# Kernel optimization log

Hardware: AMD Instinct MI355X
Metric: run time of the kernel (lower is better)

## Reference

```python
import jax, jax.numpy as jnp
import numpy as np
import math

N, M = 512, 31
INP, EMB, ATT = 64, 64, 64
NUM_RELS = 200
SELF_LOOP_IDX = NUM_RELS  # index num_rels is the self-loop relation


def setup_inputs() -> dict:
    key = jax.random.key(0)
    ks = jax.random.split(key, 11)
    s_w = 1.0 / math.sqrt(EMB)
    return {
        "h": jax.random.normal(ks[0], (N, INP), jnp.float32),
        "msg": jax.random.normal(ks[1], (N, M, EMB), jnp.float32),
        "msg_type": jax.random.randint(ks[2], (N, M), 0, NUM_RELS, jnp.int32),
        "r_label_node": jax.random.randint(ks[3], (N,), 0, NUM_RELS, jnp.int32),
        "r_label_msg": jax.random.randint(ks[4], (N, M), 0, NUM_RELS, jnp.int32),
        "W_self": jax.random.normal(ks[5], (INP, EMB), jnp.float32) * s_w,
        "Q": jax.random.normal(ks[6], (NUM_RELS + 1, EMB, ATT), jnp.float32) * s_w,
        "K": jax.random.normal(ks[7], (NUM_RELS + 1, EMB, ATT), jnp.float32) * s_w,
        "V": jax.random.normal(ks[8], (NUM_RELS + 1, EMB, ATT), jnp.float32) * s_w,
        "ffn_w": jax.random.normal(ks[9], (ATT, EMB), jnp.float32) * s_w,
        "ffn_b": jnp.zeros((EMB,), jnp.float32),
    }


def reference(h, msg, msg_type, r_label_node, r_label_msg, W_self, Q, K, V, ffn_w, ffn_b):
    curr = h @ W_self                                        # [N, EMB]
    x = jnp.concatenate([curr[:, None, :], msg], axis=1)     # [N, M+1, EMB]
    qv_idx = jnp.concatenate([r_label_node[:, None], r_label_msg], axis=1)  # [N, M+1]
    self_col = jnp.full((x.shape[0], 1), SELF_LOOP_IDX, msg_type.dtype)
    k_idx = jnp.concatenate([self_col, msg_type], axis=1)    # [N, M+1]
    # relation-indexed per-token projection weights (irregular gather)
    q = jnp.einsum("nme,nmea->nma", x, Q[qv_idx])            # [N, M+1, ATT]
    k = jnp.einsum("nme,nmea->nma", x, K[k_idx])             # [N, M+1, ATT]
    v = jnp.einsum("nme,nmea->nma", x, V[qv_idx])            # [N, M+1, ATT]
    scores = jnp.einsum("nqa,nka->nqk", q, k) / math.sqrt(ATT)
    # NOTE: original code applies softmax over dim=1 (the query axis)
    att = jax.nn.softmax(scores, axis=1)                     # [N, M+1, M+1]
    pooled = jnp.einsum("nqk,nka->nqa", att, v)[:, 0]        # [N, ATT]
    return pooled @ ffn_w + ffn_b                            # [N, EMB]
```

## Files before the change

kernel.cpp:

```cpp
#include <hip/hip_runtime.h>
#include <math.h>

#define NN 512
#define MM 31
#define TT 32
#define EE 64
#define NREL 200
#define NMAT 201
#define SELF_LOOP 200
#define QCAP 192
#define NT 6
#define WSTR 72
#define CPAD 32

typedef short  short8 __attribute__((ext_vector_type(8)));
typedef float  f32x4  __attribute__((ext_vector_type(4)));

__device__ __forceinline__ unsigned short f2bf(float f) {
    union { float f; unsigned int u; } a; a.f = f;
    unsigned int r = a.u + 0x7FFFu + ((a.u >> 16) & 1u);
    return (unsigned short)(r >> 16);
}
__device__ __forceinline__ float bf2f(unsigned short u) {
    union { unsigned int u; float f; } a; a.u = ((unsigned int)u) << 16;
    return a.f;
}

__global__ __launch_bounds__(256) void prep_convert_kernel(
    const float* __restrict__ h, const float* __restrict__ W_self,
    const float* __restrict__ Q, const float* __restrict__ K,
    const float* __restrict__ V,
    const int* __restrict__ msg_type, const int* __restrict__ r_label_node,
    const int* __restrict__ r_label_msg, const float* __restrict__ msg,
    int* __restrict__ cnt_q, int* __restrict__ cnt_k,
    int* __restrict__ list_q, int* __restrict__ list_k,
    unsigned short* __restrict__ wt_q, unsigned short* __restrict__ wt_k,
    unsigned short* __restrict__ wt_v,
    unsigned short* __restrict__ msg_bf, unsigned short* __restrict__ curr_bf,
    unsigned short* __restrict__ k_bf)
{
    const int bid = blockIdx.x, tid = threadIdx.x;

    if (bid < 3 * NMAT) {
        const int r   = bid % NMAT;
        const int mat = bid / NMAT;
        const float* src = (mat == 0 ? Q : mat == 1 ? K : V) + (size_t)r * EE * EE;
        unsigned short* dst = (mat == 0 ? wt_q : mat == 1 ? wt_k : wt_v)
                              + (size_t)r * EE * EE;
        __shared__ unsigned short t_s[EE * WSTR];
        {
            const int e = tid >> 2, aseg = (tid & 3) * 16;
            const float4* s4 = (const float4*)(src + e * EE + aseg);
            float4 f0 = s4[0], f1 = s4[1], f2 = s4[2], f3 = s4[3];
            unsigned short b[16] = {
                f2bf(f0.x), f2bf(f0.y), f2bf(f0.z), f2bf(f0.w),
                f2bf(f1.x), f2bf(f1.y), f2bf(f1.z), f2bf(f1.w),
                f2bf(f2.x), f2bf(f2.y), f2bf(f2.z), f2bf(f2.w),
                f2bf(f3.x), f2bf(f3.y), f2bf(f3.z), f2bf(f3.w) };
            unsigned short* d = &t_s[e * WSTR + aseg];
            *(short8*)d = *(short8*)&b[0];
            *(short8*)(d + 8) = *(short8*)&b[8];
        }
        __syncthreads();
        {
            const int a = tid >> 2, eseg = (tid & 3) * 16;
            unsigned short o[16];
#pragma unroll
            for (int j = 0; j < 16; ++j)
                o[j] = t_s[(eseg + j) * WSTR + a];
            unsigned short* d = dst + a * EE + eseg;
            *(short8*)d = *(short8*)&o[0];
            *(short8*)(d + 8) = *(short8*)&o[8];
        }
        return;
    }

    const int n = bid - 3 * NMAT;

    if (tid < MM) {
        int j  = n * MM + tid;
        int rl = r_label_msg[j];
        int p  = atomicAdd(&cnt_q[rl * CPAD], 1);
        if (p < QCAP) list_q[rl * QCAP + p] = n * TT + tid + 1;
        int mt = msg_type[j];
        int p2 = atomicAdd(&cnt_k[mt * CPAD], 1);
        if (p2 < QCAP) list_k[mt * QCAP + p2] = n * TT + tid + 1;
    } else if (tid == 63) {
        int r = r_label_node[n];
        int p = atomicAdd(&cnt_q[r * CPAD], 1);
        if (p < QCAP) list_q[r * QCAP + p] = n * TT;
    }

    if (tid < MM * EE / 8) {
        const float4* s4 = (const float4*)(msg + (size_t)n * MM * EE) + tid * 2;
        float4 f0 = s4[0], f1 = s4[1];
        unsigned short b[8] = { f2bf(f0.x), f2bf(f0.y), f2bf(f0.z), f2bf(f0.w),
                                f2bf(f1.x), f2bf(f1.y), f2bf(f1.z), f2bf(f1.w) };
        *(short8*)(msg_bf + (size_t)n * MM * EE + tid * 8) = *(short8*)b;
    }

    __shared__ float c_s[EE];
    if (tid < EE) {
        const float* hrow = h + n * EE;
        float acc = 0.f;
#pragma unroll 8
        for (int e = 0; e < EE; ++e)
            acc = fmaf(hrow[e], W_self[e * EE + tid], acc);
        curr_bf[n * EE + tid] = f2bf(acc);
        c_s[tid] = acc;
    }
    __syncthreads();
    if (tid < EE) {
        const float* K200 = K + (size_t)SELF_LOOP * EE * EE;
        float k0 = 0.f;
#pragma unroll 8
        for (int e = 0; e < EE; ++e)
            k0 = fmaf(c_s[e], K200[e * EE + tid], k0);
        k_bf[(size_t)n * TT * EE + tid] = f2bf(k0);
    }
}

__global__ __launch_bounds__(256) void proj_tile_kernel(
    const unsigned short* __restrict__ curr_bf,
    const unsigned short* __restrict__ msg_bf,
    const unsigned short* __restrict__ wt_q,
    const unsigned short* __restrict__ wt_k,
    const unsigned short* __restrict__ wt_v,
    const int* __restrict__ cnt_q, const int* __restrict__ cnt_k,
    const int* __restrict__ list_q, const int* __restrict__ list_k,
    unsigned short* __restrict__ q_bf, unsigned short* __restrict__ k_bf,
    unsigned short* __restrict__ v_bf)
{
    const int r    = blockIdx.x / NT;
    const int tile = blockIdx.x % NT;
    const int tid  = threadIdx.x;
    const int lane = tid & 63;
    const int wave = tid >> 6;
    const int col  = lane & 15;
    const int quad = lane >> 4;

    const int nq = min(cnt_q[r * CPAD], QCAP);
    const int nk = min(cnt_k[r * CPAD], QCAP);
    const int q0 = tile * 32;
    const bool do_q = q0 < nq;
    const bool do_k = q0 < nk;
    if (!do_q && !do_k) return;

    __shared__ unsigned short wq_s[EE * WSTR];
    __shared__ unsigned short wk_s[EE * WSTR];
    __shared__ unsigned short wv_s[EE * WSTR];
    __shared__ unsigned short x_s[64 * WSTR];
    __shared__ int tq_s[32], tk_s[32];

    {
        const int a = tid >> 2, seg = (tid & 3) * 16;
        const size_t go = (size_t)r * EE * EE + a * EE + seg;
        const int lo = a * WSTR + seg;
        if (do_q) {
            short8 w0 = *(const short8*)(wt_q + go);
            short8 w1 = *(const short8*)(wt_q + go + 8);
            *(short8*)&wq_s[lo] = w0; *(short8*)&wq_s[lo + 8] = w1;
            short8 v0 = *(const short8*)(wt_v + go);
            short8 v1 = *(const short8*)(wt_v + go + 8);
            *(short8*)&wv_s[lo] = v0; *(short8*)&wv_s[lo + 8] = v1;
        }
        if (do_k) {
            short8 k0_ = *(const short8*)(wt_k + go);
            short8 k1_ = *(const short8*)(wt_k + go + 8);
            *(short8*)&wk_s[lo] = k0_; *(short8*)&wk_s[lo + 8] = k1_;
        }
    }

    if (tid < 32) {
        tq_s[tid] = (do_q && q0 + tid < nq) ? list_q[r * QCAP + q0 + tid] : -1;
    } else if (tid < 64) {
        int i = tid - 32;
        tk_s[i] = (do_k && q0 + i < nk) ? list_k[r * QCAP + q0 + i] : -1;
    }

    {
        const int row = tid >> 2;
        const int seg = (tid & 3) * 16;
        const bool qside = row < 32;
        const int li = qside ? (q0 + row) : (q0 + row - 32);
        const bool valid = qside ? (do_q && li < nq) : (do_k && li < nk);
        if (valid) {
            int token = qside ? list_q[r * QCAP + li] : list_k[r * QCAP + li];
            int n = token >> 5, t = token & 31;
            const unsigned short* src = (t == 0)
                ? (curr_bf + n * EE)
                : (msg_bf + ((size_t)n * MM + (t - 1)) * EE);
            short8 s0 = *(const short8*)(src + seg);
            short8 s1 = *(const short8*)(src + seg + 8);
            unsigned short* d = &x_s[row * WSTR + seg];
            *(short8*)d = s0; *(short8*)(d + 8) = s1;
        }
    }
    __syncthreads();

    if (do_q) {
        const int mtile = wave & 1;
        const unsigned short* w_s = (wave >> 1) ? wv_s : wq_s;
        unsigned short* outp = (wave >> 1) ? v_bf : q_bf;
        const int m = mtile * 16 + col;
        f32x4 acc[4] = {{0,0,0,0},{0,0,0,0},{0,0,0,0},{0,0,0,0}};
#pragma unroll
        for (int kk = 0; kk < 2; ++kk) {
            short8 af = *(const short8*)&x_s[m * WSTR + kk * 32 + quad * 8];
#pragma unroll
            for (int nt = 0; nt < 4; ++nt) {
                short8 bf = *(const short8*)&w_s[(nt * 16 + col) * WSTR + kk * 32 + quad * 8];
                acc[nt] = __builtin_amdgcn_mfma_f32_16x16x32_bf16(af, bf, acc[nt], 0, 0, 0);
            }
        }
#pragma unroll
        for (int nt = 0; nt < 4; ++nt)
#pragma unroll
            for (int reg = 0; reg < 4; ++reg) {
                int rrow = mtile * 16 + quad * 4 + reg;
                int token = tq_s[rrow];
                if (token >= 0)
                    outp[(size_t)token * EE + nt * 16 + col] = f2bf(acc[nt][reg]);
            }
    }

    if (do_k) {
        const int mtile = wave & 1;
        const int nh = wave >> 1;
        const int m = 32 + mtile * 16 + col;
        f32x4 acc[2] = {{0,0,0,0},{0,0,0,0}};
#pragma unroll
        for (int kk = 0; kk < 2; ++kk) {
            short8 af = *(const short8*)&x_s[m * WSTR + kk * 32 + quad * 8];
#pragma unroll
            for (int j = 0; j < 2; ++j) {
                int nt = nh * 2 + j;
                short8 bf = *(const short8*)&wk_s[(nt * 16 + col) * WSTR + kk * 32 + quad * 8];
                acc[j] = __builtin_amdgcn_mfma_f32_16x16x32_bf16(af, bf, acc[j], 0, 0, 0);
            }
        }
#pragma unroll
        for (int j = 0; j < 2; ++j)
#pragma unroll
            for (int reg = 0; reg < 4; ++reg) {
                int rrow = mtile * 16 + quad * 4 + reg;
                int token = tk_s[rrow];
                if (token >= 0)
                    k_bf[(size_t)token * EE + (nh * 2 + j) * 16 + col] = f2bf(acc[j][reg]);
            }
    }
}

__global__ __launch_bounds__(256) void attn_kernel(
    const unsigned short* __restrict__ q_bf,
    const unsigned short* __restrict__ k_bf,
    const unsigned short* __restrict__ v_bf,
    const float* __restrict__ ffn_w, const float* __restrict__ ffn_b,
    float* __restrict__ out)
{
    const int n = blockIdx.x, tid = threadIdx.x;
    __shared__ float q_s[TT][68], k_s[TT][68], v_s[TT][68];
    __shared__ float s_s[TT][TT + 1];
    __shared__ float att0[TT];
    __shared__ float pooled[EE];

    {
        const int row = tid >> 3, c8 = (tid & 7) * 8;
        const size_t go = (size_t)n * TT * EE + row * EE + c8;
        short8 q8 = *(const short8*)(q_bf + go);
        short8 k8 = *(const short8*)(k_bf + go);
        short8 v8 = *(const short8*)(v_bf + go);
#pragma unroll
        for (int j = 0; j < 8; ++j) {
            q_s[row][c8 + j] = bf2f(((unsigned short*)&q8)[j]);
            k_s[row][c8 + j] = bf2f(((unsigned short*)&k8)[j]);
            v_s[row][c8 + j] = bf2f(((unsigned short*)&v8)[j]);
        }
    }
    __syncthreads();

    {
        const int ki = tid & 31;
        for (int qi = tid >> 5; qi < TT; qi += 8) {
            const float4* qp = (const float4*)&q_s[qi][0];
            const float4* kp = (const float4*)&k_s[ki][0];
            float acc = 0.f;
            for (int e4 = 0; e4 < EE / 4; ++e4) {
                float4 a = qp[e4], b = kp[e4];
                acc += a.x * b.x + a.y * b.y + a.z * b.z + a.w * b.w;
            }
            s_s[qi][ki] = acc * 0.125f;
        }
    }
    __syncthreads();

    if (tid < TT) {
        float mx = -INFINITY;
        for (int qi = 0; qi < TT; ++qi) mx = fmaxf(mx, s_s[qi][tid]);
        float sum = 0.f;
        for (int qi = 0; qi < TT; ++qi) sum += __expf(s_s[qi][tid] - mx);
        att0[tid] = __expf(s_s[0][tid] - mx) / sum;
    }
    __syncthreads();

    if (tid < EE) {
        float acc = 0.f;
        for (int ki = 0; ki < TT; ++ki)
            acc = fmaf(att0[ki], v_s[ki][tid], acc);
        pooled[tid] = acc;
    }
    __syncthreads();

    if (tid < EE) {
        float acc = ffn_b[tid];
        for (int a = 0; a < EE; ++a)
            acc = fmaf(pooled[a], ffn_w[a * EE + tid], acc);
        out[n * EE + tid] = acc;
    }
}

extern "C" void kernel_launch(void* const* d_in, const int* in_sizes, int n_in,
                              void* d_out, int out_size, void* d_ws, size_t ws_size,
                              hipStream_t stream) {
    const float* h            = (const float*)d_in[0];
    const float* msg          = (const float*)d_in[1];
    const int*   msg_type     = (const int*)  d_in[2];
    const int*   r_label_node = (const int*)  d_in[3];
    const int*   r_label_msg  = (const int*)  d_in[4];
    const float* W_self       = (const float*)d_in[5];
    const float* Q            = (const float*)d_in[6];
    const float* K            = (const float*)d_in[7];
    const float* V            = (const float*)d_in[8];
    const float* ffn_w        = (const float*)d_in[9];
    const float* ffn_b        = (const float*)d_in[10];
    float*       out          = (float*)d_out;

    int* cnt_q  = (int*)d_ws;
    int* cnt_k  = cnt_q + NREL * CPAD;
    int* list_q = cnt_k + NREL * CPAD;
    int* list_k = list_q + NREL * QCAP;
    unsigned short* wt_q = (unsigned short*)(list_k + NREL * QCAP);
    unsigned short* wt_k = wt_q + (size_t)NMAT * EE * EE;
    unsigned short* wt_v = wt_k + (size_t)NMAT * EE * EE;
    unsigned short* msg_bf  = wt_v + (size_t)NMAT * EE * EE;
    unsigned short* curr_bf = msg_bf + (size_t)NN * MM * EE;
    unsigned short* q_bf = curr_bf + NN * EE;
    unsigned short* k_bf = q_bf + (size_t)NN * TT * EE;
    unsigned short* v_bf = k_bf + (size_t)NN * TT * EE;

    hipMemsetAsync(cnt_q, 0, 2 * NREL * CPAD * sizeof(int), stream);
    prep_convert_kernel<<<3 * NMAT + NN, 256, 0, stream>>>(
        h, W_self, Q, K, V, msg_type, r_label_node, r_label_msg, msg,
        cnt_q, cnt_k, list_q, list_k, wt_q, wt_k, wt_v,
        msg_bf, curr_bf, k_bf);
    proj_tile_kernel<<<NREL * NT, 256, 0, stream>>>(
        curr_bf, msg_bf, wt_q, wt_k, wt_v, cnt_q, cnt_k, list_q, list_k,
        q_bf, k_bf, v_bf);
    attn_kernel<<<NN, 256, 0, stream>>>(q_bf, k_bf, v_bf, ffn_w, ffn_b, out);
}
```

Measured before the change: 107.7 us.

## Bucket relation lists in 16 dedicated blocks with shared-memory atomics, drop memset

Building the per-relation token lists moves out of the per-node blocks, which used global atomics, and into 16 extra blocks. Each of these scans all labels and owns the relations whose low four bits match its block index, counting with LDS atomics. Counts are written directly at the end, so the hipMemsetAsync launch goes away. In exchange, each of the 16 blocks reads the full label arrays, and those blocks may finish after the conversion work and sit on the critical path.

```diff
diff --git a/kernel.cpp b/kernel.cpp
--- a/kernel.cpp
+++ b/kernel.cpp
@@ -12,6 +12,7 @@
 #define NT 6
 #define WSTR 72
 #define CPAD 32
+#define SB 16
 
 typedef short  short8 __attribute__((ext_vector_type(8)));
 typedef float  f32x4  __attribute__((ext_vector_type(4)));
@@ -41,9 +42,45 @@
 {
     const int bid = blockIdx.x, tid = threadIdx.x;
 
-    if (bid < 3 * NMAT) {
-        const int r   = bid % NMAT;
-        const int mat = bid / NMAT;
+    if (bid < SB) {
+        const int b = bid;
+        __shared__ int lcq[NREL], lck[NREL];
+        if (tid < NREL) { lcq[tid] = 0; lck[tid] = 0; }
+        __syncthreads();
+
+        for (int j = tid; j < NN * MM; j += 256) {
+            int rl = r_label_msg[j];
+            int mt = msg_type[j];
+            int n = j / MM, m = j - n * MM;
+            int token = n * TT + m + 1;
+            if ((rl & 15) == b) {
+                int p = atomicAdd(&lcq[rl], 1);
+                if (p < QCAP) list_q[rl * QCAP + p] = token;
+            }
+            if ((mt & 15) == b) {
+                int p = atomicAdd(&lck[mt], 1);
+                if (p < QCAP) list_k[mt * QCAP + p] = token;
+            }
+        }
+        for (int i = tid; i < NN; i += 256) {
+            int r = r_label_node[i];
+            if ((r & 15) == b) {
+                int p = atomicAdd(&lcq[r], 1);
+                if (p < QCAP) list_q[r * QCAP + p] = i * TT;
+            }
+        }
+        __syncthreads();
+        if (tid < NREL && (tid & 15) == b) {
+            cnt_q[tid * CPAD] = lcq[tid];
+            cnt_k[tid * CPAD] = lck[tid];
+        }
+        return;
+    }
+
+    if (bid < SB + 3 * NMAT) {
+        const int cb  = bid - SB;
+        const int r   = cb % NMAT;
+        const int mat = cb / NMAT;
         const float* src = (mat == 0 ? Q : mat == 1 ? K : V) + (size_t)r * EE * EE;
         unsigned short* dst = (mat == 0 ? wt_q : mat == 1 ? wt_k : wt_v)
                               + (size_t)r * EE * EE;
@@ -52,14 +89,14 @@
             const int e = tid >> 2, aseg = (tid & 3) * 16;
             const float4* s4 = (const float4*)(src + e * EE + aseg);
             float4 f0 = s4[0], f1 = s4[1], f2 = s4[2], f3 = s4[3];
-            unsigned short b[16] = {
+            unsigned short bb[16] = {
                 f2bf(f0.x), f2bf(f0.y), f2bf(f0.z), f2bf(f0.w),
                 f2bf(f1.x), f2bf(f1.y), f2bf(f1.z), f2bf(f1.w),
                 f2bf(f2.x), f2bf(f2.y), f2bf(f2.z), f2bf(f2.w),
                 f2bf(f3.x), f2bf(f3.y), f2bf(f3.z), f2bf(f3.w) };
             unsigned short* d = &t_s[e * WSTR + aseg];
-            *(short8*)d = *(short8*)&b[0];
-            *(short8*)(d + 8) = *(short8*)&b[8];
+            *(short8*)d = *(short8*)&bb[0];
+            *(short8*)(d + 8) = *(short8*)&bb[8];
         }
         __syncthreads();
         {
@@ -75,21 +112,7 @@
         return;
     }
 
-    const int n = bid - 3 * NMAT;
-
-    if (tid < MM) {
-        int j  = n * MM + tid;
-        int rl = r_label_msg[j];
-        int p  = atomicAdd(&cnt_q[rl * CPAD], 1);
-        if (p < QCAP) list_q[rl * QCAP + p] = n * TT + tid + 1;
-        int mt = msg_type[j];
-        int p2 = atomicAdd(&cnt_k[mt * CPAD], 1);
-        if (p2 < QCAP) list_k[mt * QCAP + p2] = n * TT + tid + 1;
-    } else if (tid == 63) {
-        int r = r_label_node[n];
-        int p = atomicAdd(&cnt_q[r * CPAD], 1);
-        if (p < QCAP) list_q[r * QCAP + p] = n * TT;
-    }
+    const int n = bid - SB - 3 * NMAT;
 
     if (tid < MM * EE / 8) {
         const float4* s4 = (const float4*)(msg + (size_t)n * MM * EE) + tid * 2;
@@ -348,8 +371,7 @@
     unsigned short* k_bf = q_bf + (size_t)NN * TT * EE;
     unsigned short* v_bf = k_bf + (size_t)NN * TT * EE;
 
-    hipMemsetAsync(cnt_q, 0, 2 * NREL * CPAD * sizeof(int), stream);
-    prep_convert_kernel<<<3 * NMAT + NN, 256, 0, stream>>>(
+    prep_convert_kernel<<<SB + 3 * NMAT + NN, 256, 0, stream>>>(
         h, W_self, Q, K, V, msg_type, r_label_node, r_label_msg, msg,
         cnt_q, cnt_k, list_q, list_k, wt_q, wt_k, wt_v,
         msg_bf, curr_bf, k_bf);
```

New measurement: 132.4 us. +23.0%, slower.
